# Optimization experiments

Hardware: AMD Instinct MI355X
Metric: run time of the kernel (lower is better)

Reference implementation:

```python
import jax, jax.numpy as jnp
import numpy as np

ALPHA = 0.2  # LeakyReLU negative slope
OUT_FEATURES = 64


def dsn2(t):
    # Closed-form doubly-stochastic normalization for one [N, N] slice.
    n = t.shape[0]
    rs = t.sum(axis=1, keepdims=True)          # [N, 1] row sums
    cs = t.sum(axis=0, keepdims=True)          # [1, N] col sums
    lamb = jnp.maximum(rs.max(), cs.max())
    r = n * lamb - t.sum()
    tt = t + (lamb * lamb - lamb * (rs + cs) + rs * cs) / r
    ttm = tt / tt.sum(axis=0)[0]               # divide by first column-sum (scalar), per original
    return jnp.where(t > 0, ttm, t)


def setup_inputs() -> dict:
    key = jax.random.key(0)
    k1, k2, k3, k4 = jax.random.split(key, 4)
    N, P, IN, OUT = 3072, 4, 256, OUT_FEATURES
    h = jax.random.normal(k1, (N, IN), dtype=jnp.float32)
    edge_attr = jax.random.uniform(k2, (P, N, N), dtype=jnp.float32)
    W = jax.random.normal(k3, (IN, OUT), dtype=jnp.float32) * 0.1
    a = jax.random.normal(k4, (2 * OUT, 1), dtype=jnp.float32) * 0.1
    return {"h": h, "edge_attr": edge_attr, "W": W, "a": a}


def reference(h, edge_attr, W, a):
    F = OUT_FEATURES
    Wh = h @ W                                   # [N, F]
    Wh1 = Wh @ a[:F, :]                          # [N, 1]
    Wh2 = Wh @ a[F:, :]                          # [N, 1]
    e = jax.nn.leaky_relu(Wh1 + Wh2.T, negative_slope=ALPHA)  # [N, N]
    e = e * edge_attr                            # [P, N, N]
    attention = jax.vmap(dsn2)(e)                # [P, N, N]
    h_prime = jnp.einsum('pij,jf->pif', attention, Wh)  # [P, N, F]
    # concat=True: cat along feature dim -> [N, P*F]
    N = h.shape[0]
    h_cat = jnp.transpose(h_prime, (1, 0, 2)).reshape(N, -1)
    return jax.nn.elu(h_cat), e
```

## Files before the change

### kernel.cpp

```cpp
#include <hip/hip_runtime.h>
#include <math.h>

#define NN 3072
#define PP 4
#define INF_ 256
#define FF 64
#define LEAK 0.2f
#define KB2 384
#define KS 4
#define KCH (NN / KS)
#define PNF (PP * NN * FF)

#define WH1_OFF  0
#define WH2_OFF  (WH1_OFF + NN)
#define RS_OFF   (WH2_OFF + NN)
#define CS_OFF   (RS_OFF + PP * NN)
#define U_OFF    (CS_OFF + PP * NN)
#define V_OFF    (U_OFF + PP * NN)
#define SCAL_OFF (V_OFF + PP * NN)
#define WHT_OFF  (SCAL_OFF + 8)
#define CP_OFF   (WHT_OFF + (NN * FF) / 2)

typedef short short8 __attribute__((ext_vector_type(8)));
typedef float floatx4 __attribute__((ext_vector_type(4)));

__device__ inline unsigned short f2bf(float x) {
    unsigned u = __float_as_uint(x);
    return (unsigned short)((u + 0x7FFFu + ((u >> 16) & 1u)) >> 16);
}

__global__ __launch_bounds__(64) void k1_gemm(const float* __restrict__ h,
                                              const float* __restrict__ W,
                                              const float* __restrict__ a,
                                              float* __restrict__ ws) {
    int row = blockIdx.x;
    int f = threadIdx.x;
    __shared__ float hrow[INF_];
    ((float4*)hrow)[f] = ((const float4*)(h + (size_t)row * INF_))[f];
    __syncthreads();
    float acc = 0.f;
#pragma unroll 8
    for (int k = 0; k < INF_; ++k) acc = fmaf(hrow[k], W[k * FF + f], acc);
    unsigned short* whT = (unsigned short*)(ws + WHT_OFF);
    whT[(size_t)f * NN + row] = f2bf(acc);
    float s1 = acc * a[f];
    float s2 = acc * a[FF + f];
#pragma unroll
    for (int off = 32; off > 0; off >>= 1) {
        s1 += __shfl_down(s1, off);
        s2 += __shfl_down(s2, off);
    }
    if (f == 0) { ws[WH1_OFF + row] = s1; ws[WH2_OFF + row] = s2; }
}

__global__ __launch_bounds__(256) void k2_e(const float* __restrict__ edge,
                                            float* __restrict__ e_out,
                                            float* __restrict__ ws) {
    int p = blockIdx.y;
    int row0 = blockIdx.x * 8;
    int tid = threadIdx.x;
    const float* Wh1 = ws + WH1_OFF;
    const float4* Wh2v = (const float4*)(ws + WH2_OFF);
    float4 wv[3];
#pragma unroll
    for (int c = 0; c < 3; ++c) wv[c] = Wh2v[c * 256 + tid];
    float colAcc[12];
#pragma unroll
    for (int i = 0; i < 12; ++i) colAcc[i] = 0.f;
    float racc8[8];
    __shared__ float rowpart[8][4];
    const size_t slice = (size_t)p * NN * NN;
    const float4* ein = (const float4*)(edge + slice + (size_t)row0 * NN);
    float4* eout = (float4*)(e_out + slice + (size_t)row0 * NN);
    float4 c0 = ein[tid], c1 = ein[256 + tid], c2 = ein[512 + tid];
#pragma unroll
    for (int r = 0; r < 8; ++r) {
        float4 n0, n1, n2;
        if (r < 7) {
            const float4* nx = ein + (size_t)(r + 1) * 768;
            n0 = nx[tid]; n1 = nx[256 + tid]; n2 = nx[512 + tid];
        }
        float w1 = Wh1[row0 + r];
        float4* eor = eout + (size_t)r * 768;
        float racc = 0.f;
        float4 ea, w, ev;
        float b;
        ea = c0; w = wv[0];
        b = w1 + w.x; b = b > 0.f ? b : LEAK * b; ev.x = b * ea.x;
        b = w1 + w.y; b = b > 0.f ? b : LEAK * b; ev.y = b * ea.y;
        b = w1 + w.z; b = b > 0.f ? b : LEAK * b; ev.z = b * ea.z;
        b = w1 + w.w; b = b > 0.f ? b : LEAK * b; ev.w = b * ea.w;
        eor[tid] = ev;
        colAcc[0] += ev.x; colAcc[1] += ev.y; colAcc[2] += ev.z; colAcc[3] += ev.w;
        racc += (ev.x + ev.y) + (ev.z + ev.w);
        ea = c1; w = wv[1];
        b = w1 + w.x; b = b > 0.f ? b : LEAK * b; ev.x = b * ea.x;
        b = w1 + w.y; b = b > 0.f ? b : LEAK * b; ev.y = b * ea.y;
        b = w1 + w.z; b = b > 0.f ? b : LEAK * b; ev.z = b * ea.z;
        b = w1 + w.w; b = b > 0.f ? b : LEAK * b; ev.w = b * ea.w;
        eor[256 + tid] = ev;
        colAcc[4] += ev.x; colAcc[5] += ev.y; colAcc[6] += ev.z; colAcc[7] += ev.w;
        racc += (ev.x + ev.y) + (ev.z + ev.w);
        ea = c2; w = wv[2];
        b = w1 + w.x; b = b > 0.f ? b : LEAK * b; ev.x = b * ea.x;
        b = w1 + w.y; b = b > 0.f ? b : LEAK * b; ev.y = b * ea.y;
        b = w1 + w.z; b = b > 0.f ? b : LEAK * b; ev.z = b * ea.z;
        b = w1 + w.w; b = b > 0.f ? b : LEAK * b; ev.w = b * ea.w;
        eor[512 + tid] = ev;
        colAcc[8] += ev.x; colAcc[9] += ev.y; colAcc[10] += ev.z; colAcc[11] += ev.w;
        racc += (ev.x + ev.y) + (ev.z + ev.w);
        racc8[r] = racc;
        c0 = n0; c1 = n1; c2 = n2;
    }
#pragma unroll
    for (int r = 0; r < 8; ++r) {
        float racc = racc8[r];
#pragma unroll
        for (int off = 32; off > 0; off >>= 1) racc += __shfl_down(racc, off);
        if ((tid & 63) == 0) rowpart[r][tid >> 6] = racc;
    }
    __syncthreads();
    if (tid < 32) {
        float vv = rowpart[tid >> 2][tid & 3];
        vv += __shfl_down(vv, 2);
        vv += __shfl_down(vv, 1);
        if ((tid & 3) == 0) ws[RS_OFF + p * NN + row0 + (tid >> 2)] = vv;
    }
    float4* cp = (float4*)(ws + CP_OFF + (size_t)(p * KB2 + blockIdx.x) * NN);
#pragma unroll
    for (int c = 0; c < 3; ++c) {
        float4 cv;
        cv.x = colAcc[c * 4 + 0]; cv.y = colAcc[c * 4 + 1];
        cv.z = colAcc[c * 4 + 2]; cv.w = colAcc[c * 4 + 3];
        cp[c * 256 + tid] = cv;
    }
}

__global__ __launch_bounds__(256) void k3a_red(float* __restrict__ ws) {
    int p = blockIdx.y;
    int col = blockIdx.x * 64 + (threadIdx.x & 63);
    int chunk = threadIdx.x >> 6;
    const float* cp = ws + CP_OFF + (size_t)p * KB2 * NN + (size_t)chunk * 96 * NN + col;
    float s = 0.f;
#pragma unroll 8
    for (int b = 0; b < 96; ++b) s += cp[(size_t)b * NN];
    __shared__ float sred[4][64];
    sred[chunk][threadIdx.x & 63] = s;
    __syncthreads();
    if (threadIdx.x < 64) {
        float t = sred[0][threadIdx.x] + sred[1][threadIdx.x] +
                  sred[2][threadIdx.x] + sred[3][threadIdx.x];
        ws[CS_OFF + p * NN + col] = t;
    }
}

__global__ __launch_bounds__(256) void k3b_scal(float* __restrict__ ws) {
    int p = blockIdx.x;
    int tid = threadIdx.x;
    const float* rs = ws + RS_OFF + p * NN;
    const float* cs = ws + CS_OFF + p * NN;
    float mx = -3.4e38f, sum = 0.f;
    for (int i = tid; i < NN; i += 256) {
        float rv = rs[i], cv = cs[i];
        mx = fmaxf(mx, fmaxf(rv, cv));
        sum += rv;
    }
#pragma unroll
    for (int off = 32; off > 0; off >>= 1) {
        mx = fmaxf(mx, __shfl_down(mx, off));
        sum += __shfl_down(sum, off);
    }
    __shared__ float smx[4], ssum[4];
    __shared__ float s_lamb, s_invlr;
    if ((tid & 63) == 0) { smx[tid >> 6] = mx; ssum[tid >> 6] = sum; }
    __syncthreads();
    if (tid == 0) {
        float lamb = fmaxf(fmaxf(smx[0], smx[1]), fmaxf(smx[2], smx[3]));
        float T = ssum[0] + ssum[1] + ssum[2] + ssum[3];
        float r = (float)NN * lamb - T;
        s_lamb = lamb;
        s_invlr = 1.f / (r * lamb);
        ws[SCAL_OFF + p] = 1.f / lamb;
    }
    __syncthreads();
    float lamb = s_lamb, invlr = s_invlr;
    for (int i = tid; i < NN; i += 256) {
        ws[U_OFF + p * NN + i] = (lamb - rs[i]) * invlr;
        ws[V_OFF + p * NN + i] = lamb - cs[i];
    }
}

__global__ __launch_bounds__(256) void k4_mfma(const float* __restrict__ e_in,
                                               float* __restrict__ ws) {
    int p = blockIdx.y;
    int z = blockIdx.z;
    int row0 = blockIdx.x * 32;
    int tid = threadIdx.x;
    int lane = tid & 63, wid = tid >> 6;

    __shared__ unsigned short sA[2][32 * 64];
    __shared__ unsigned short sB[2][64 * 64];

    const unsigned short* whT = (const unsigned short*)(ws + WHT_OFF);
    const float* u = ws + U_OFF + p * NN;
    const float* v = ws + V_OFF + p * NN;
    float invl = ws[SCAL_OFF + p];
    const float* eslice = e_in + (size_t)p * NN * NN;

    const int ar = tid >> 3, acg = tid & 7;
    const int bfr = tid >> 2, bkg = tid & 3;
    const float u_r = u[row0 + ar];
    const float* erow = eslice + (size_t)(row0 + ar) * NN;
    const unsigned short* wrow = whT + (size_t)bfr * NN;
    const int aswL = ((acg >> 1) ^ (ar & 7)) * 8 + (acg & 1) * 4;
    const int aswH = (((acg >> 1) + 4) ^ (ar & 7)) * 8 + (acg & 1) * 4;
    const int bswL = (bkg ^ (bfr & 7)) * 8;
    const int bswH = ((bkg + 4) ^ (bfr & 7)) * 8;

    const int mrow = lane & 15, kq = lane >> 4;
    const int rt = wid & 1, ft = (wid >> 1) * 2;
    const int arow = rt * 16 + mrow;
    const int sw = mrow & 7;

    floatx4 acc0, acc1;
#pragma unroll
    for (int i = 0; i < 4; ++i) { acc0[i] = 0.f; acc1[i] = 0.f; }

    float4 eL, eH, vL, vH;
    int4 bLd, bHd;
    auto LD = [&](int k0) {
        const float4* ep = (const float4*)(erow + k0);
        eL = ep[acg]; eH = ep[acg + 8];
        const float4* vp = (const float4*)(v + k0);
        vL = vp[acg]; vH = vp[acg + 8];
        const int4* wp = (const int4*)(wrow + k0);
        bLd = wp[bkg]; bHd = wp[bkg + 4];
    };
    auto ST = [&](int b) {
        float a0 = eL.x > 0.f ? fmaf(u_r, vL.x, eL.x * invl) : eL.x;
        float a1 = eL.y > 0.f ? fmaf(u_r, vL.y, eL.y * invl) : eL.y;
        float a2 = eL.z > 0.f ? fmaf(u_r, vL.z, eL.z * invl) : eL.z;
        float a3 = eL.w > 0.f ? fmaf(u_r, vL.w, eL.w * invl) : eL.w;
        float a4 = eH.x > 0.f ? fmaf(u_r, vH.x, eH.x * invl) : eH.x;
        float a5 = eH.y > 0.f ? fmaf(u_r, vH.y, eH.y * invl) : eH.y;
        float a6 = eH.z > 0.f ? fmaf(u_r, vH.z, eH.z * invl) : eH.z;
        float a7 = eH.w > 0.f ? fmaf(u_r, vH.w, eH.w * invl) : eH.w;
        int2 lo, hi;
        lo.x = (int)f2bf(a0) | ((int)f2bf(a1) << 16);
        lo.y = (int)f2bf(a2) | ((int)f2bf(a3) << 16);
        hi.x = (int)f2bf(a4) | ((int)f2bf(a5) << 16);
        hi.y = (int)f2bf(a6) | ((int)f2bf(a7) << 16);
        *(int2*)&sA[b][ar * 64 + aswL] = lo;
        *(int2*)&sA[b][ar * 64 + aswH] = hi;
        *(int4*)&sB[b][bfr * 64 + bswL] = bLd;
        *(int4*)&sB[b][bfr * 64 + bswH] = bHd;
    };
    auto MM = [&](int b) {
        short8 a0 = *(const short8*)&sA[b][arow * 64 + (kq ^ sw) * 8];
        short8 a1 = *(const short8*)&sA[b][arow * 64 + ((4 + kq) ^ sw) * 8];
        int f0 = (ft * 16 + mrow) * 64;
        int f1 = f0 + 16 * 64;
        short8 b00 = *(const short8*)&sB[b][f0 + (kq ^ sw) * 8];
        short8 b01 = *(const short8*)&sB[b][f0 + ((4 + kq) ^ sw) * 8];
        short8 b10 = *(const short8*)&sB[b][f1 + (kq ^ sw) * 8];
        short8 b11 = *(const short8*)&sB[b][f1 + ((4 + kq) ^ sw) * 8];
        acc0 = __builtin_amdgcn_mfma_f32_16x16x32_bf16(a0, b00, acc0, 0, 0, 0);
        acc0 = __builtin_amdgcn_mfma_f32_16x16x32_bf16(a1, b01, acc0, 0, 0, 0);
        acc1 = __builtin_amdgcn_mfma_f32_16x16x32_bf16(a0, b10, acc1, 0, 0, 0);
        acc1 = __builtin_amdgcn_mfma_f32_16x16x32_bf16(a1, b11, acc1, 0, 0, 0);
    };

    const int kbase = z * KCH;
    const int NSTEP = KCH / 64;
    LD(kbase);
    ST(0);
    __syncthreads();
    int buf = 0;
    for (int step = 0; step < NSTEP; ++step) {
        if (step + 1 < NSTEP) {
            LD(kbase + (step + 1) * 64);
            MM(buf);
            ST(buf ^ 1);
            __syncthreads();
        } else {
            MM(buf);
        }
        buf ^= 1;
    }
    float* part = ws + CP_OFF + (size_t)z * PNF + (size_t)p * NN * FF + (size_t)row0 * FF;
#pragma unroll
    for (int r = 0; r < 4; ++r) {
        int crow = rt * 16 + kq * 4 + r;
        part[crow * FF + ft * 16 + mrow] = acc0[r];
        part[crow * FF + (ft + 1) * 16 + mrow] = acc1[r];
    }
}

__global__ __launch_bounds__(256) void k5_red(const float* __restrict__ ws,
                                              float* __restrict__ out0) {
    int i = blockIdx.x * 256 + threadIdx.x;
    const float* part = ws + CP_OFF;
    float s = part[i] + part[PNF + i] + part[2 * PNF + i] + part[3 * (size_t)PNF + i];
    s = s > 0.f ? s : (expf(s) - 1.0f);
    int f = i & 63;
    int p = i / (NN * FF);
    int n = (i - p * NN * FF) >> 6;
    out0[(size_t)n * (PP * FF) + p * FF + f] = s;
}

extern "C" void kernel_launch(void* const* d_in, const int* in_sizes, int n_in,
                              void* d_out, int out_size, void* d_ws, size_t ws_size,
                              hipStream_t stream) {
    const float* h    = (const float*)d_in[0];
    const float* edge = (const float*)d_in[1];
    const float* W    = (const float*)d_in[2];
    const float* a    = (const float*)d_in[3];
    float* out0  = (float*)d_out;
    float* e_out = out0 + (size_t)NN * PP * FF;
    float* ws = (float*)d_ws;

    k1_gemm<<<NN, 64, 0, stream>>>(h, W, a, ws);
    k2_e<<<dim3(NN / 8, PP), 256, 0, stream>>>(edge, e_out, ws);
    k3a_red<<<dim3(NN / 64, PP), 256, 0, stream>>>(ws);
    k3b_scal<<<PP, 256, 0, stream>>>(ws);
    k4_mfma<<<dim3(NN / 32, PP, KS), 256, 0, stream>>>(e_out, ws);
    k5_red<<<PNF / 256, 256, 0, stream>>>(ws, out0);
}
```

Baseline: 356.4 us.

## Double k2 rows per block and restructure k4 prefetch with two register sets

```diff
diff --git a/kernel.cpp b/kernel.cpp
--- a/kernel.cpp
+++ b/kernel.cpp
@@ -6,7 +6,7 @@
 #define INF_ 256
 #define FF 64
 #define LEAK 0.2f
-#define KB2 384
+#define KB2 192
 #define KS 4
 #define KCH (NN / KS)
 #define PNF (PP * NN * FF)
@@ -57,7 +57,7 @@
                                             float* __restrict__ e_out,
                                             float* __restrict__ ws) {
     int p = blockIdx.y;
-    int row0 = blockIdx.x * 8;
+    int row0 = blockIdx.x * 16;
     int tid = threadIdx.x;
     const float* Wh1 = ws + WH1_OFF;
     const float4* Wh2v = (const float4*)(ws + WH2_OFF);
@@ -67,16 +67,16 @@
     float colAcc[12];
 #pragma unroll
     for (int i = 0; i < 12; ++i) colAcc[i] = 0.f;
-    float racc8[8];
-    __shared__ float rowpart[8][4];
+    float racc16[16];
+    __shared__ float rowpart[16][4];
     const size_t slice = (size_t)p * NN * NN;
     const float4* ein = (const float4*)(edge + slice + (size_t)row0 * NN);
     float4* eout = (float4*)(e_out + slice + (size_t)row0 * NN);
     float4 c0 = ein[tid], c1 = ein[256 + tid], c2 = ein[512 + tid];
 #pragma unroll
-    for (int r = 0; r < 8; ++r) {
+    for (int r = 0; r < 16; ++r) {
         float4 n0, n1, n2;
-        if (r < 7) {
+        if (r < 15) {
             const float4* nx = ein + (size_t)(r + 1) * 768;
             n0 = nx[tid]; n1 = nx[256 + tid]; n2 = nx[512 + tid];
         }
@@ -109,18 +109,18 @@
         eor[512 + tid] = ev;
         colAcc[8] += ev.x; colAcc[9] += ev.y; colAcc[10] += ev.z; colAcc[11] += ev.w;
         racc += (ev.x + ev.y) + (ev.z + ev.w);
-        racc8[r] = racc;
+        racc16[r] = racc;
         c0 = n0; c1 = n1; c2 = n2;
     }
 #pragma unroll
-    for (int r = 0; r < 8; ++r) {
-        float racc = racc8[r];
+    for (int r = 0; r < 16; ++r) {
+        float racc = racc16[r];
 #pragma unroll
         for (int off = 32; off > 0; off >>= 1) racc += __shfl_down(racc, off);
         if ((tid & 63) == 0) rowpart[r][tid >> 6] = racc;
     }
     __syncthreads();
-    if (tid < 32) {
+    if (tid < 64) {
         float vv = rowpart[tid >> 2][tid & 3];
         vv += __shfl_down(vv, 2);
         vv += __shfl_down(vv, 1);
@@ -140,10 +140,10 @@
     int p = blockIdx.y;
     int col = blockIdx.x * 64 + (threadIdx.x & 63);
     int chunk = threadIdx.x >> 6;
-    const float* cp = ws + CP_OFF + (size_t)p * KB2 * NN + (size_t)chunk * 96 * NN + col;
+    const float* cp = ws + CP_OFF + (size_t)p * KB2 * NN + (size_t)chunk * 48 * NN + col;
     float s = 0.f;
 #pragma unroll 8
-    for (int b = 0; b < 96; ++b) s += cp[(size_t)b * NN];
+    for (int b = 0; b < 48; ++b) s += cp[(size_t)b * NN];
     __shared__ float sred[4][64];
     sred[chunk][threadIdx.x & 63] = s;
     __syncthreads();
@@ -226,25 +226,24 @@
 #pragma unroll
     for (int i = 0; i < 4; ++i) { acc0[i] = 0.f; acc1[i] = 0.f; }
 
-    float4 eL, eH, vL, vH;
-    int4 bLd, bHd;
-    auto LD = [&](int k0) {
+    struct LdRegs { float4 eL, eH, vL, vH; int4 bL, bH; };
+    auto LD = [&](LdRegs& R, int k0) {
         const float4* ep = (const float4*)(erow + k0);
-        eL = ep[acg]; eH = ep[acg + 8];
+        R.eL = ep[acg]; R.eH = ep[acg + 8];
         const float4* vp = (const float4*)(v + k0);
-        vL = vp[acg]; vH = vp[acg + 8];
+        R.vL = vp[acg]; R.vH = vp[acg + 8];
         const int4* wp = (const int4*)(wrow + k0);
-        bLd = wp[bkg]; bHd = wp[bkg + 4];
+        R.bL = wp[bkg]; R.bH = wp[bkg + 4];
     };
-    auto ST = [&](int b) {
-        float a0 = eL.x > 0.f ? fmaf(u_r, vL.x, eL.x * invl) : eL.x;
-        float a1 = eL.y > 0.f ? fmaf(u_r, vL.y, eL.y * invl) : eL.y;
-        float a2 = eL.z > 0.f ? fmaf(u_r, vL.z, eL.z * invl) : eL.z;
-        float a3 = eL.w > 0.f ? fmaf(u_r, vL.w, eL.w * invl) : eL.w;
-        float a4 = eH.x > 0.f ? fmaf(u_r, vH.x, eH.x * invl) : eH.x;
-        float a5 = eH.y > 0.f ? fmaf(u_r, vH.y, eH.y * invl) : eH.y;
-        float a6 = eH.z > 0.f ? fmaf(u_r, vH.z, eH.z * invl) : eH.z;
-        float a7 = eH.w > 0.f ? fmaf(u_r, vH.w, eH.w * invl) : eH.w;
+    auto ST = [&](const LdRegs& R, int b) {
+        float a0 = R.eL.x > 0.f ? fmaf(u_r, R.vL.x, R.eL.x * invl) : R.eL.x;
+        float a1 = R.eL.y > 0.f ? fmaf(u_r, R.vL.y, R.eL.y * invl) : R.eL.y;
+        float a2 = R.eL.z > 0.f ? fmaf(u_r, R.vL.z, R.eL.z * invl) : R.eL.z;
+        float a3 = R.eL.w > 0.f ? fmaf(u_r, R.vL.w, R.eL.w * invl) : R.eL.w;
+        float a4 = R.eH.x > 0.f ? fmaf(u_r, R.vH.x, R.eH.x * invl) : R.eH.x;
+        float a5 = R.eH.y > 0.f ? fmaf(u_r, R.vH.y, R.eH.y * invl) : R.eH.y;
+        float a6 = R.eH.z > 0.f ? fmaf(u_r, R.vH.z, R.eH.z * invl) : R.eH.z;
+        float a7 = R.eH.w > 0.f ? fmaf(u_r, R.vH.w, R.eH.w * invl) : R.eH.w;
         int2 lo, hi;
         lo.x = (int)f2bf(a0) | ((int)f2bf(a1) << 16);
         lo.y = (int)f2bf(a2) | ((int)f2bf(a3) << 16);
@@ -252,8 +251,8 @@
         hi.y = (int)f2bf(a6) | ((int)f2bf(a7) << 16);
         *(int2*)&sA[b][ar * 64 + aswL] = lo;
         *(int2*)&sA[b][ar * 64 + aswH] = hi;
-        *(int4*)&sB[b][bfr * 64 + bswL] = bLd;
-        *(int4*)&sB[b][bfr * 64 + bswH] = bHd;
+        *(int4*)&sB[b][bfr * 64 + bswL] = R.bL;
+        *(int4*)&sB[b][bfr * 64 + bswH] = R.bH;
     };
     auto MM = [&](int b) {
         short8 a0 = *(const short8*)&sA[b][arow * 64 + (kq ^ sw) * 8];
@@ -272,20 +271,22 @@
 
     const int kbase = z * KCH;
     const int NSTEP = KCH / 64;
-    LD(kbase);
-    ST(0);
-    __syncthreads();
-    int buf = 0;
-    for (int step = 0; step < NSTEP; ++step) {
-        if (step + 1 < NSTEP) {
-            LD(kbase + (step + 1) * 64);
-            MM(buf);
-            ST(buf ^ 1);
+    LdRegs RA, RB;
+    LD(RA, kbase);
+    ST(RA, 0);
+    LD(RB, kbase + 64);
+    __syncthreads();
+    for (int s = 0; s < NSTEP; s += 2) {
+        MM(0);
+        ST(RB, 1);
+        if (s + 2 < NSTEP) LD(RA, kbase + (s + 2) * 64);
+        __syncthreads();
+        MM(1);
+        if (s + 2 < NSTEP) {
+            ST(RA, 0);
+            if (s + 3 < NSTEP) LD(RB, kbase + (s + 3) * 64);
             __syncthreads();
-        } else {
-            MM(buf);
         }
-        buf ^= 1;
     }
     float* part = ws + CP_OFF + (size_t)z * PNF + (size_t)p * NN * FF + (size_t)row0 * FF;
 #pragma unroll
@@ -320,7 +321,7 @@
     float* ws = (float*)d_ws;
 
     k1_gemm<<<NN, 64, 0, stream>>>(h, W, a, ws);
-    k2_e<<<dim3(NN / 8, PP), 256, 0, stream>>>(edge, e_out, ws);
+    k2_e<<<dim3(NN / 16, PP), 256, 0, stream>>>(edge, e_out, ws);
     k3a_red<<<dim3(NN / 64, PP), 256, 0, stream>>>(ws);
     k3b_scal<<<PP, 256, 0, stream>>>(ws);
     k4_mfma<<<dim3(NN / 32, PP, KS), 256, 0, stream>>>(e_out, ws);
```

Measured after the change: 340.2 us. 1.05x faster.
